# Performance work log

Measured on AMD Instinct MI355X. Metric: run time of the kernel, lower is better.

## Reference

```python
import jax, jax.numpy as jnp
import numpy as np

K = 5            # srn kernel size (kernels[0])
EPSILON = 1e-3   # epsilons -> SRN additive noise scale
BN_EPS = 1e-5
NUM_SLICES = 3
OUT_CH = 64
CLASSES = 5


def _unfold(x, k):
    # torch.nn.Unfold, padding=0: (B, C*k*k, L), channel-major then (kh, kw) row-major
    B, C, H, W = x.shape
    Ho, Wo = H - k + 1, W - k + 1
    cols = jnp.stack([x[:, :, i:i + Ho, j:j + Wo]
                      for i in range(k) for j in range(k)], axis=2)  # (B,C,k*k,Ho,Wo)
    return cols.reshape(B, C * k * k, Ho * Wo), Ho, Wo


def _bn(x, g, b):
    # BatchNorm2d in training mode: batch statistics, biased variance
    m = x.mean((0, 2, 3), keepdims=True)
    v = x.var((0, 2, 3), keepdims=True)
    return (x - m) * jax.lax.rsqrt(v + BN_EPS) * g[None, :, None, None] + b[None, :, None, None]


def _conv(x, w, b):
    y = jax.lax.conv_general_dilated(x, w, (1, 1), 'VALID',
                                     dimension_numbers=('NCHW', 'OIHW', 'NCHW'))
    return y + b[None, :, None, None]


def _avgpool(x, s):
    B, C, H, W = x.shape
    return x.reshape(B, C, H // s, s, W // s, s).mean((3, 5))


def _maxpool(x, s):
    B, C, H, W = x.shape
    return x.reshape(B, C, H // s, s, W // s, s).max((3, 5))


def _srn(x, srn_w):
    B = x.shape[0]
    y, Ho, Wo = _unfold(x, K)                               # (B, n, L)
    y = y + EPSILON * jax.random.normal(jax.random.key(42), y.shape, y.dtype)
    gg = jnp.std(y, axis=1, ddof=1, keepdims=True)          # torch.std is unbiased
    y = y / gg
    O, C, _, _, S = srn_w.shape
    n = C * K * K
    X = srn_w.reshape(O, n, S)
    X = jnp.concatenate([jnp.ones((O, n, 1), X.dtype), X], axis=2)   # (O, n, S+1)
    Xcov = jnp.einsum('onf,ong->ofg', X, X)                 # X^T X, (O, 4, 4)
    Xinv = jnp.linalg.inv(Xcov)
    M = jnp.einsum('ofg,ong->ofn', Xinv, X)
    Wc = jnp.einsum('ofn,bnl->bofl', M, y)
    pred = jnp.einsum('onf,bofl->bonl', X, Wc)              # fitted values (B,O,n,L)
    err = jnp.mean((y[:, None] - pred) ** 2, axis=2)        # (B,O,L)
    err = err.reshape(B, O, Ho, Wo)
    A = (jnp.exp(-err) - np.exp(-1.0)) / (1.0 - np.exp(-1.0))
    return A - 0.5


def setup_inputs() -> dict:
    key = jax.random.key(0)
    ks = jax.random.split(key, 12)
    x = jax.random.normal(ks[0], (4, 3, 64, 64), jnp.float32)
    # xavier-style init scaled up for numerical stability of the small-matrix inverse
    srn_w = 0.05 * jax.random.normal(ks[1], (OUT_CH, 3, K, K, NUM_SLICES), jnp.float32)
    conv2_w = 0.05 * jax.random.normal(ks[2], (128, 64, 3, 3), jnp.float32)
    conv2_b = 0.01 * jax.random.normal(ks[3], (128,), jnp.float32)
    conv3_w = 0.05 * jax.random.normal(ks[4], (128, 128, 3, 3), jnp.float32)
    conv3_b = 0.01 * jax.random.normal(ks[5], (128,), jnp.float32)
    conv4_w = 0.05 * jax.random.normal(ks[6], (128, 128, 3, 3), jnp.float32)
    conv4_b = 0.01 * jax.random.normal(ks[7], (128,), jnp.float32)
    bn1_g = jnp.ones((64,), jnp.float32); bn1_b = jnp.zeros((64,), jnp.float32)
    bn2_g = jnp.ones((128,), jnp.float32); bn2_b = jnp.zeros((128,), jnp.float32)
    bn3_g = jnp.ones((128,), jnp.float32); bn3_b = jnp.zeros((128,), jnp.float32)
    bn4_g = jnp.ones((128,), jnp.float32); bn4_b = jnp.zeros((128,), jnp.float32)
    fc2_w = 0.05 * jax.random.normal(ks[8], (CLASSES, 128, 1, 1), jnp.float32)
    fc2_b = 0.01 * jax.random.normal(ks[9], (CLASSES,), jnp.float32)
    return dict(x=x, srn_w=srn_w, conv2_w=conv2_w, conv2_b=conv2_b,
                conv3_w=conv3_w, conv3_b=conv3_b, conv4_w=conv4_w, conv4_b=conv4_b,
                bn1_g=bn1_g, bn1_b=bn1_b, bn2_g=bn2_g, bn2_b=bn2_b,
                bn3_g=bn3_g, bn3_b=bn3_b, bn4_g=bn4_g, bn4_b=bn4_b,
                fc2_w=fc2_w, fc2_b=fc2_b)


def reference(x, srn_w, conv2_w, conv2_b, conv3_w, conv3_b, conv4_w, conv4_b,
              bn1_g, bn1_b, bn2_g, bn2_b, bn3_g, bn3_b, bn4_g, bn4_b,
              fc2_w, fc2_b):
    h = _srn(x, srn_w)                                      # (B,64,60,60)
    h = _avgpool(h, 2)
    h = _bn(h, bn1_g, bn1_b)
    h = jax.nn.relu(_bn(_conv(h, conv2_w, conv2_b), bn2_g, bn2_b))
    h = _avgpool(h, 2)
    h = jax.nn.relu(_bn(_conv(h, conv3_w, conv3_b), bn3_g, bn3_b))
    h = _maxpool(h, 2)
    h = jax.nn.relu(_bn(_conv(h, conv4_w, conv4_b), bn4_g, bn4_b))
    h = _maxpool(h, 4)                                      # (B,128,1,1)
    flat = h.reshape(h.shape[0], -1)                        # (B,128)
    return flat @ fc2_w.reshape(CLASSES, -1).T + fc2_b      # 1x1 conv == matmul
```

## Files before the change

kernel.cpp:

```cpp
#include <hip/hip_runtime.h>
#include <math.h>

__device__ __align__(16) float g_w2p[9 * 2304 * 4];
__device__ __align__(16) float g_w3p[17 * 2304 * 4];
__device__ __align__(16) float g_w4p[8 * 4608 * 4];
__device__ __align__(16) float g_h1[4 * 30 * 30 * 64];
__device__ __align__(16) float g_h2[4 * 14 * 14 * 4 * 128];
__device__ __align__(16) float g_h3[4 * 6 * 6 * 4 * 128];
__device__ __align__(16) float g_h4[4 * 16 * 128];

__global__ __launch_bounds__(256) void k_srn(const float* __restrict__ x,
                                             const float* __restrict__ srn_w,
                                             const float* __restrict__ w2,
                                             float* __restrict__ stats) {
    __shared__ __align__(16) float wlds[64 * 244];
    __shared__ float xsm[648];
    __shared__ float part[2 * 15 * 66];
    __shared__ float redS[256], redQ[256];
    int bid = blockIdx.x, t = threadIdx.x;
    int b = bid / 60, rem = bid % 60, r = rem >> 1, ch = rem & 1;

    for (int j = bid * 256 + t; j < 73728; j += 240 * 256) {
        int c = j & 3, s4 = j >> 2;
        int sl = s4 % 36, tmp = s4 / 36, oc_l = tmp & 63, blk = tmp >> 6;
        int it = blk & 3, ocg = blk >> 2;
        int kw = sl % 3, icq = (sl / 3) & 3, kh = sl / 12;
        int ic = it * 16 + icq * 4 + c;
        g_w2p[j] = w2[((ocg * 64 + oc_l) * 64 + ic) * 9 + kh * 3 + kw];
    }

    float4 wr[15];
#pragma unroll
    for (int k = 0; k < 15; k++) {
        int i4 = k * 256 + t;
        if (i4 < 3600) wr[k] = ((const float4*)srn_w)[i4];
    }
    float xr[3];
#pragma unroll
    for (int k = 0; k < 3; k++) {
        int i = t + k * 256;
        if (i < 648) {
            int c = i / 216, rm = i % 216, rr = rm / 36, col = rm % 36;
            int gc = ch * 30 + col; if (gc > 63) gc = 63;
            xr[k] = x[((b * 3 + c) * 64 + (2 * r + rr)) * 64 + gc];
        }
    }
#pragma unroll
    for (int k = 0; k < 15; k++) {
        int i4 = k * 256 + t;
        if (i4 < 3600) {
            float v4[4] = { wr[k].x, wr[k].y, wr[k].z, wr[k].w };
#pragma unroll
            for (int e = 0; e < 4; e++) {
                int i = i4 * 4 + e, o = i / 225, jj = i % 225;
                wlds[o * 244 + (jj / 15) * 16 + (jj % 15)] = v4[e];
            }
        }
    }
#pragma unroll
    for (int k = 0; k < 3; k++) { int i = t + k * 256; if (i < 648) xsm[i] = xr[k]; }
    __syncthreads();

    int w = t >> 6, o = t & 63;
    int rw = w & 1, cq = w >> 1, base = cq * 16;

    float z1[16], z2[16], z3[16], s[16], q[16];
#pragma unroll
    for (int i = 0; i < 16; i++) { z1[i]=0; z2[i]=0; z3[i]=0; s[i]=0; q[i]=0; }

    for (int c = 0; c < 3; c++) {
#pragma unroll
        for (int kh = 0; kh < 5; kh++) {
            float xv[20];
#pragma unroll
            for (int k = 0; k < 20; k++) xv[k] = xsm[(c * 6 + rw + kh) * 36 + base + k];
            float wf[16];
            const float* wp = &wlds[o * 244 + (c * 5 + kh) * 16];
            *(float4*)&wf[0]  = *(const float4*)&wp[0];
            *(float4*)&wf[4]  = *(const float4*)&wp[4];
            *(float4*)&wf[8]  = *(const float4*)&wp[8];
            *(float4*)&wf[12] = *(const float4*)&wp[12];
#pragma unroll
            for (int kw = 0; kw < 5; kw++) {
                float w1 = wf[kw * 3], w2v = wf[kw * 3 + 1], w3v = wf[kw * 3 + 2];
#pragma unroll
                for (int i = 0; i < 16; i++) {
                    float v = xv[kw + i];
                    s[i] += v; q[i] += v * v;
                    z1[i] += w1 * v; z2[i] += w2v * v; z3[i] += w3v * v;
                }
            }
        }
    }

    float gm[16];
    {
        float c01=0,c02=0,c03=0,c11=0,c12=0,c13=0,c22=0,c23=0,c33=0;
#pragma unroll
        for (int row = 0; row < 15; row++) {
            float wf[16];
            const float* wp = &wlds[o * 244 + row * 16];
            *(float4*)&wf[0]  = *(const float4*)&wp[0];
            *(float4*)&wf[4]  = *(const float4*)&wp[4];
            *(float4*)&wf[8]  = *(const float4*)&wp[8];
            *(float4*)&wf[12] = *(const float4*)&wp[12];
#pragma unroll
            for (int kw = 0; kw < 5; kw++) {
                float w1 = wf[kw*3], w2v = wf[kw*3+1], w3v = wf[kw*3+2];
                c01 += w1; c02 += w2v; c03 += w3v;
                c11 += w1*w1; c12 += w1*w2v; c13 += w1*w3v;
                c22 += w2v*w2v; c23 += w2v*w3v; c33 += w3v*w3v;
            }
        }
        float A[4][8];
        A[0][0]=75.f; A[0][1]=c01; A[0][2]=c02; A[0][3]=c03;
        A[1][0]=c01;  A[1][1]=c11; A[1][2]=c12; A[1][3]=c13;
        A[2][0]=c02;  A[2][1]=c12; A[2][2]=c22; A[2][3]=c23;
        A[3][0]=c03;  A[3][1]=c13; A[3][2]=c23; A[3][3]=c33;
#pragma unroll
        for (int i = 0; i < 4; i++)
#pragma unroll
            for (int j = 0; j < 4; j++) A[i][4 + j] = (i == j) ? 1.f : 0.f;
#pragma unroll
        for (int p = 0; p < 4; p++) {
            float ip = 1.f / A[p][p];
#pragma unroll
            for (int j = 0; j < 8; j++) A[p][j] *= ip;
#pragma unroll
            for (int i = 0; i < 4; i++) if (i != p) {
                float f = A[i][p];
#pragma unroll
                for (int j = 0; j < 8; j++) A[i][j] -= f * A[p][j];
            }
        }
#pragma unroll
        for (int i = 0; i < 4; i++)
#pragma unroll
            for (int j = 0; j < 4; j++) gm[i * 4 + j] = A[i][4 + j];
    }

    const float C1 = 0.36787944117144233f;
    const float INV = 1.5819767068693265f;
#pragma unroll
    for (int pp = 0; pp < 8; pp++) {
        int pl = cq * 8 + pp;
        if (pl < 15) {
            float aa = 0.f;
#pragma unroll
            for (int e = 0; e < 2; e++) {
                int i = 2 * pp + e;
                float sum = s[i], sq = q[i];
                float gg2 = (sq - sum * sum * (1.f / 75.f)) * (1.f / 74.f);
                float zf[4] = { sum, z1[i], z2[i], z3[i] };
                float qf = 0.f;
#pragma unroll
                for (int f = 0; f < 4; f++) {
                    float acc = 0.f;
#pragma unroll
                    for (int h = 0; h < 4; h++) acc += gm[f * 4 + h] * zf[h];
                    qf += acc * zf[f];
                }
                float err = (sq - qf) / (75.f * gg2);
                aa += (expf(-err) - C1) * INV - 0.5f;
            }
            part[(rw * 15 + pl) * 66 + o] = 0.25f * aa;
        }
    }
    __syncthreads();

    int j2 = t >> 6;
    float ps = 0.f, pq = 0.f;
    for (int pl = j2; pl < 15; pl += 4) {
        float v = part[pl * 66 + o] + part[(15 + pl) * 66 + o];
        g_h1[((b * 30 + r) * 30 + ch * 15 + pl) * 64 + o] = v;
        ps += v; pq += v * v;
    }
    redS[t] = ps; redQ[t] = pq;
    __syncthreads();
    if (t < 64) {
        atomicAdd(&stats[t],      redS[t] + redS[64 + t] + redS[128 + t] + redS[192 + t]);
        atomicAdd(&stats[64 + t], redQ[t] + redQ[64 + t] + redQ[128 + t] + redQ[192 + t]);
    }
}

__global__ __launch_bounds__(256) void k_conv2(const float* __restrict__ w3,
                                               const float* __restrict__ g1,
                                               const float* __restrict__ b1,
                                               float* __restrict__ stats) {
    __shared__ __align__(16) float ws[64 * 148];
    __shared__ __align__(16) float xs[3 * 16 * 64];
    __shared__ float redS[256], redQ[256];
    int blk = blockIdx.x, t = threadIdx.x;
    int b = blk / 112, rem = blk % 112, oh = rem >> 2, sub = rem & 3;
    int owh = sub >> 1, ocg = sub & 1;
    int oc_l = t & 63, qtr = t >> 6;
    int now = (qtr < 2) ? 4 : 3;
    int lowb = (qtr < 2) ? qtr * 4 : 8 + (qtr - 2) * 3;

    for (int j = blk * 256 + t; j < 147456; j += 448 * 256) {
        int c = j & 3, s4 = j >> 2;
        int sl = s4 % 36, tmp = s4 / 36, oc2 = tmp & 63, bk = tmp >> 6;
        int it = bk & 7, og = bk >> 3;
        int kw = sl % 3, icq = (sl / 3) & 3, kh = sl / 12;
        int ic = it * 16 + icq * 4 + c;
        g_w3p[j] = w3[((og * 64 + oc2) * 128 + ic) * 9 + kh * 3 + kw];
    }

    {
        int icb = (t & 15) * 4;
        float4 S = *(const float4*)&stats[icb], Q = *(const float4*)&stats[64 + icb];
        float4 G4 = *(const float4*)&g1[icb], B4 = *(const float4*)&b1[icb];
        float scv[4], shv[4];
        float mm[4] = { S.x, S.y, S.z, S.w }, qq[4] = { Q.x, Q.y, Q.z, Q.w };
        float gg[4] = { G4.x, G4.y, G4.z, G4.w }, bb[4] = { B4.x, B4.y, B4.z, B4.w };
#pragma unroll
        for (int c = 0; c < 4; c++) {
            float m = mm[c] * (1.f / 3600.f);
            float v = qq[c] * (1.f / 3600.f) - m * m;
            scv[c] = gg[c] * rsqrtf(v + 1e-5f);
            shv[c] = bb[c] - m * scv[c];
        }
        int px = t >> 4, ic4 = t & 15;
        float4 xr[3];
#pragma unroll
        for (int k = 0; k < 3; k++)
            xr[k] = ((const float4*)g_h1)[((b * 30 + oh + k) * 30 + owh * 14 + px) * 16 + ic4];
        const float4* wsrc0 = (const float4*)g_w2p;
        float4 wreg[9];
#pragma unroll
        for (int k = 0; k < 9; k++) wreg[k] = wsrc0[(ocg * 4) * 2304 + k * 256 + t];
#pragma unroll
        for (int k = 0; k < 3; k++) {
            float4 v;
            v.x = xr[k].x * scv[0] + shv[0]; v.y = xr[k].y * scv[1] + shv[1];
            v.z = xr[k].z * scv[2] + shv[2]; v.w = xr[k].w * scv[3] + shv[3];
            *(float4*)&xs[((k * 16 + px) * 16 + ic4) * 4] = v;
        }
#pragma unroll
        for (int k = 0; k < 9; k++) {
            int idx = k * 256 + t;
            *(float4*)&ws[(idx / 36) * 148 + (idx % 36) * 4] = wreg[k];
        }
    }
    __syncthreads();

    float acc[4] = {0, 0, 0, 0};
    const float4* wsrc = (const float4*)g_w2p + (ocg * 4) * 2304;
    for (int it = 0; it < 4; ++it) {
        float4 wreg[9];
        if (it < 3) {
#pragma unroll
            for (int k = 0; k < 9; k++) wreg[k] = wsrc[(it + 1) * 2304 + k * 256 + t];
        }
#pragma unroll 1
        for (int icq = 0; icq < 4; icq++) {
            int xoff = it * 16 + icq * 4;
#pragma unroll
            for (int kh = 0; kh < 3; kh++) {
                const float* wb = &ws[oc_l * 148 + (kh * 4 + icq) * 12];
                float4 w0 = *(const float4*)&wb[0];
                float4 w1 = *(const float4*)&wb[4];
                float4 w2v = *(const float4*)&wb[8];
                const float* xrow = &xs[(kh * 16 + lowb) * 64 + xoff];
                float4 x0 = *(const float4*)&xrow[0];
                float4 x1 = *(const float4*)&xrow[64];
#pragma unroll
                for (int i = 0; i < 4; i++) {
                    if (i < now) {
                        float4 x2 = *(const float4*)&xrow[(i + 2) * 64];
                        acc[i] += w0.x * x0.x + w0.y * x0.y + w0.z * x0.z + w0.w * x0.w
                                + w1.x * x1.x + w1.y * x1.y + w1.z * x1.z + w1.w * x1.w
                                + w2v.x * x2.x + w2v.y * x2.y + w2v.z * x2.z + w2v.w * x2.w;
                        x0 = x1; x1 = x2;
                    }
                }
            }
        }
        if (it < 3) {
            __syncthreads();
#pragma unroll
            for (int k = 0; k < 9; k++) {
                int idx = k * 256 + t;
                *(float4*)&ws[(idx / 36) * 148 + (idx % 36) * 4] = wreg[k];
            }
            __syncthreads();
        }
    }
    int oc = ocg * 64 + oc_l;
    float ps = 0.f, pq = 0.f;
#pragma unroll
    for (int i = 0; i < 4; i++) {
        if (i < now) {
            int ow = owh * 14 + lowb + i;
            g_h2[(((b * 14 + (oh >> 1)) * 14 + (ow >> 1)) * 4 + (oh & 1) * 2 + (ow & 1)) * 128 + oc] = acc[i];
            ps += acc[i]; pq += acc[i] * acc[i];
        }
    }
    redS[t] = ps; redQ[t] = pq;
    __syncthreads();
    if (t < 64) {
        atomicAdd(&stats[128 + ocg * 64 + t], redS[t] + redS[64 + t] + redS[128 + t] + redS[192 + t]);
        atomicAdd(&stats[256 + ocg * 64 + t], redQ[t] + redQ[64 + t] + redQ[128 + t] + redQ[192 + t]);
    }
}

__global__ __launch_bounds__(256) void k_conv3(const float* __restrict__ w4,
                                               const float* __restrict__ g2,
                                               const float* __restrict__ b2,
                                               float* __restrict__ stats) {
    __shared__ __align__(16) float ws[64 * 148];
    __shared__ __align__(16) float xs[3 * 8 * 128];
    __shared__ float redS[256], redQ[256];
    int blk = blockIdx.x, t = threadIdx.x;
    int b = blk / 48, rem = blk % 48, oh = rem >> 2, sub = rem & 3;
    int owh = sub >> 1, ocg = sub & 1;
    int oc_l = t & 63, qtr = t >> 6;
    int now = (qtr < 2) ? 2 : 1;
    int lowb = (qtr < 2) ? qtr * 2 : 4 + (qtr - 2);

    for (int j = blk * 256 + t; j < 147456; j += 192 * 256) {
        int c = j & 3, s4 = j >> 2;
        int sl = s4 % 72, tmp = s4 / 72, oc2 = tmp & 15, blkq = tmp >> 4;
        int icq = blkq & 3, og = blkq >> 2;
        int kw = sl % 3, icb2 = (sl / 3) & 7, kh = sl / 24;
        int ic = icq * 32 + icb2 * 4 + c;
        g_w4p[j] = w4[((og * 16 + oc2) * 128 + ic) * 9 + kh * 3 + kw];
    }

    {
        int icb = (t & 31) * 4;
        float4 S = *(const float4*)&stats[128 + icb], Q = *(const float4*)&stats[256 + icb];
        float4 G4 = *(const float4*)&g2[icb], B4 = *(const float4*)&b2[icb];
        float scv[4], shv[4];
        float mm[4] = { S.x, S.y, S.z, S.w }, qq[4] = { Q.x, Q.y, Q.z, Q.w };
        float gg[4] = { G4.x, G4.y, G4.z, G4.w }, bb[4] = { B4.x, B4.y, B4.z, B4.w };
#pragma unroll
        for (int c = 0; c < 4; c++) {
            float m = mm[c] * (1.f / 3136.f);
            float v = qq[c] * (1.f / 3136.f) - m * m;
            scv[c] = gg[c] * rsqrtf(v + 1e-5f);
            shv[c] = bb[c] - m * scv[c];
        }
        const float4* wsrc0 = (const float4*)g_w3p;
        float4 wreg[9];
#pragma unroll
        for (int k = 0; k < 9; k++) wreg[k] = wsrc0[(ocg * 8) * 2304 + k * 256 + t];
        int px = (t >> 5) & 7, ic4 = t & 31;
        float4 pa[3], pb[3], pc[3], pd[3];
#pragma unroll
        for (int k = 0; k < 3; k++) {
            const float4* p0 = (const float4*)&g_h2[(((b * 14 + oh + k) * 14 + owh * 6 + px) * 4) * 128 + ic4 * 4];
            pa[k] = p0[0]; pb[k] = p0[32]; pc[k] = p0[64]; pd[k] = p0[96];
        }
#pragma unroll
        for (int k = 0; k < 9; k++) {
            int idx = k * 256 + t;
            *(float4*)&ws[(idx / 36) * 148 + (idx % 36) * 4] = wreg[k];
        }
#pragma unroll
        for (int k = 0; k < 3; k++) {
            float4 o4;
            o4.x = 0.25f * (fmaxf(pa[k].x * scv[0] + shv[0], 0.f) + fmaxf(pb[k].x * scv[0] + shv[0], 0.f)
                          + fmaxf(pc[k].x * scv[0] + shv[0], 0.f) + fmaxf(pd[k].x * scv[0] + shv[0], 0.f));
            o4.y = 0.25f * (fmaxf(pa[k].y * scv[1] + shv[1], 0.f) + fmaxf(pb[k].y * scv[1] + shv[1], 0.f)
                          + fmaxf(pc[k].y * scv[1] + shv[1], 0.f) + fmaxf(pd[k].y * scv[1] + shv[1], 0.f));
            o4.z = 0.25f * (fmaxf(pa[k].z * scv[2] + shv[2], 0.f) + fmaxf(pb[k].z * scv[2] + shv[2], 0.f)
                          + fmaxf(pc[k].z * scv[2] + shv[2], 0.f) + fmaxf(pd[k].z * scv[2] + shv[2], 0.f));
            o4.w = 0.25f * (fmaxf(pa[k].w * scv[3] + shv[3], 0.f) + fmaxf(pb[k].w * scv[3] + shv[3], 0.f)
                          + fmaxf(pc[k].w * scv[3] + shv[3], 0.f) + fmaxf(pd[k].w * scv[3] + shv[3], 0.f));
            *(float4*)&xs[((k * 8 + px) * 32 + ic4) * 4] = o4;
        }
    }
    __syncthreads();

    float acc[2] = {0, 0};
    const float4* wsrc = (const float4*)g_w3p + (ocg * 8) * 2304;
    for (int it = 0; it < 8; ++it) {
        float4 wreg[9];
        if (it < 7) {
#pragma unroll
            for (int k = 0; k < 9; k++) wreg[k] = wsrc[(it + 1) * 2304 + k * 256 + t];
        }
#pragma unroll 1
        for (int icq = 0; icq < 4; icq++) {
            int xoff = it * 16 + icq * 4;
#pragma unroll
            for (int kh = 0; kh < 3; kh++) {
                const float* wb = &ws[oc_l * 148 + (kh * 4 + icq) * 12];
                float4 w0 = *(const float4*)&wb[0];
                float4 w1 = *(const float4*)&wb[4];
                float4 w2v = *(const float4*)&wb[8];
                const float* xrow = &xs[(kh * 8 + lowb) * 128 + xoff];
                float4 x0 = *(const float4*)&xrow[0];
                float4 x1 = *(const float4*)&xrow[128];
#pragma unroll
                for (int i = 0; i < 2; i++) {
                    if (i < now) {
                        float4 x2 = *(const float4*)&xrow[(i + 2) * 128];
                        acc[i] += w0.x * x0.x + w0.y * x0.y + w0.z * x0.z + w0.w * x0.w
                                + w1.x * x1.x + w1.y * x1.y + w1.z * x1.z + w1.w * x1.w
                                + w2v.x * x2.x + w2v.y * x2.y + w2v.z * x2.z + w2v.w * x2.w;
                        x0 = x1; x1 = x2;
                    }
                }
            }
        }
        if (it < 7) {
            __syncthreads();
#pragma unroll
            for (int k = 0; k < 9; k++) {
                int idx = k * 256 + t;
                *(float4*)&ws[(idx / 36) * 148 + (idx % 36) * 4] = wreg[k];
            }
            __syncthreads();
        }
    }
    int oc = ocg * 64 + oc_l;
    float ps = 0.f, pq = 0.f;
#pragma unroll
    for (int i = 0; i < 2; i++) {
        if (i < now) {
            int ow = owh * 6 + lowb + i;
            g_h3[(((b * 6 + (oh >> 1)) * 6 + (ow >> 1)) * 4 + (oh & 1) * 2 + (ow & 1)) * 128 + oc] = acc[i];
            ps += acc[i]; pq += acc[i] * acc[i];
        }
    }
    redS[t] = ps; redQ[t] = pq;
    __syncthreads();
    if (t < 64) {
        atomicAdd(&stats[384 + ocg * 64 + t], redS[t] + redS[64 + t] + redS[128 + t] + redS[192 + t]);
        atomicAdd(&stats[512 + ocg * 64 + t], redQ[t] + redQ[64 + t] + redQ[128 + t] + redQ[192 + t]);
    }
}

__global__ __launch_bounds__(256) void k_conv4(const float* __restrict__ g3,
                                               const float* __restrict__ b3,
                                               float* __restrict__ stats) {
    __shared__ __align__(16) float ws[64 * 292];
    __shared__ __align__(16) float xs[3 * 6 * 128];
    __shared__ float red[256];
    int blk = blockIdx.x, t = threadIdx.x;
    int b = blk / 32, rem = blk % 32, oh = rem / 8, ocg = rem % 8;
    int oc_l = t & 15, ow = (t >> 4) & 3, icq = t >> 6;

    {
        int icb = (t & 31) * 4;
        float4 S = *(const float4*)&stats[384 + icb], Q = *(const float4*)&stats[512 + icb];
        float4 G4 = *(const float4*)&g3[icb], B4 = *(const float4*)&b3[icb];
        float scv[4], shv[4];
        float mm[4] = { S.x, S.y, S.z, S.w }, qq[4] = { Q.x, Q.y, Q.z, Q.w };
        float gg[4] = { G4.x, G4.y, G4.z, G4.w }, bb[4] = { B4.x, B4.y, B4.z, B4.w };
#pragma unroll
        for (int c = 0; c < 4; c++) {
            float m = mm[c] * (1.f / 576.f);
            float v = qq[c] * (1.f / 576.f) - m * m;
            scv[c] = gg[c] * rsqrtf(v + 1e-5f);
            shv[c] = bb[c] - m * scv[c];
        }
        const float4* wsrc = (const float4*)g_w4p + ocg * 4608;
        float4 wreg[18];
#pragma unroll
        for (int k = 0; k < 18; k++) wreg[k] = wsrc[k * 256 + t];
        float4 pa[3], pb[3], pc[3], pd[3];
#pragma unroll
        for (int k = 0; k < 3; k++) {
            int i4 = t + k * 256;
            if (i4 < 576) {
                int px = (i4 >> 5) % 6, rr = i4 / 192;
                const float4* p0 = (const float4*)&g_h3[(((b * 6 + oh + rr) * 6 + px) * 4) * 128 + (i4 & 31) * 4];
                pa[k] = p0[0]; pb[k] = p0[32]; pc[k] = p0[64]; pd[k] = p0[96];
            }
        }
#pragma unroll
        for (int k = 0; k < 18; k++) {
            int idx = k * 256 + t;
            *(float4*)&ws[(idx / 72) * 292 + (idx % 72) * 4] = wreg[k];
        }
#pragma unroll
        for (int k = 0; k < 3; k++) {
            int i4 = t + k * 256;
            if (i4 < 576) {
                float4 o4;
                o4.x = fmaxf(fmaxf(fmaxf(pa[k].x * scv[0] + shv[0], pb[k].x * scv[0] + shv[0]),
                                   fmaxf(pc[k].x * scv[0] + shv[0], pd[k].x * scv[0] + shv[0])), 0.f);
                o4.y = fmaxf(fmaxf(fmaxf(pa[k].y * scv[1] + shv[1], pb[k].y * scv[1] + shv[1]),
                                   fmaxf(pc[k].y * scv[1] + shv[1], pd[k].y * scv[1] + shv[1])), 0.f);
                o4.z = fmaxf(fmaxf(fmaxf(pa[k].z * scv[2] + shv[2], pb[k].z * scv[2] + shv[2]),
                                   fmaxf(pc[k].z * scv[2] + shv[2], pd[k].z * scv[2] + shv[2])), 0.f);
                o4.w = fmaxf(fmaxf(fmaxf(pa[k].w * scv[3] + shv[3], pb[k].w * scv[3] + shv[3]),
                                   fmaxf(pc[k].w * scv[3] + shv[3], pd[k].w * scv[3] + shv[3])), 0.f);
                *(float4*)&xs[i4 * 4] = o4;
            }
        }
    }
    __syncthreads();

    float acc = 0.f;
    const float* wbase = &ws[(icq * 16 + oc_l) * 292];
#pragma unroll 1
    for (int icbq = 0; icbq < 8; icbq++) {
#pragma unroll
        for (int kh = 0; kh < 3; kh++) {
            const float* wb = &wbase[(kh * 8 + icbq) * 12];
            float4 w0 = *(const float4*)&wb[0];
            float4 w1 = *(const float4*)&wb[4];
            float4 w2v = *(const float4*)&wb[8];
            float4 x0 = *(const float4*)&xs[(kh * 6 + ow) * 128 + icq * 32 + icbq * 4];
            float4 x1 = *(const float4*)&xs[(kh * 6 + ow + 1) * 128 + icq * 32 + icbq * 4];
            float4 x2 = *(const float4*)&xs[(kh * 6 + ow + 2) * 128 + icq * 32 + icbq * 4];
            acc += w0.x * x0.x + w0.y * x0.y + w0.z * x0.z + w0.w * x0.w
                 + w1.x * x1.x + w1.y * x1.y + w1.z * x1.z + w1.w * x1.w
                 + w2v.x * x2.x + w2v.y * x2.y + w2v.z * x2.z + w2v.w * x2.w;
        }
    }
    red[t] = acc;
    __syncthreads();
    if (t < 64) {
        float v = red[t] + red[t + 64] + red[t + 128] + red[t + 192];
        int oc = ocg * 16 + (t & 15);
        g_h4[((b * 4 + oh) * 4 + (t >> 4)) * 128 + oc] = v;
        float ps = v + __shfl_xor(v, 16);  ps += __shfl_xor(ps, 32);
        float pv = v * v;
        float pq = pv + __shfl_xor(pv, 16); pq += __shfl_xor(pq, 32);
        if (t < 16) {
            atomicAdd(&stats[640 + ocg * 16 + t], ps);
            atomicAdd(&stats[768 + ocg * 16 + t], pq);
        }
    }
}

__global__ __launch_bounds__(256) void k_final(const float* __restrict__ g4,
                                               const float* __restrict__ b4,
                                               const float* __restrict__ fcw,
                                               const float* __restrict__ fcb,
                                               const float* __restrict__ stats,
                                               float* __restrict__ out) {
    __shared__ float sc[128], sh[128];
    __shared__ float pooled[4][128];
    int t = threadIdx.x;
    if (t < 128) {
        float m = stats[640 + t] * (1.f / 64.f);
        float v = stats[768 + t] * (1.f / 64.f) - m * m;
        float rs = rsqrtf(v + 1e-5f);
        sc[t] = g4[t] * rs; sh[t] = b4[t] - m * sc[t];
    }
    __syncthreads();
    for (int item = t; item < 512; item += 256) {
        int bb = item >> 7, oc = item & 127;
        float s = sc[oc], h = sh[oc];
        float mx = 0.f;
#pragma unroll
        for (int k = 0; k < 16; k++) mx = fmaxf(mx, g_h4[(bb * 16 + k) * 128 + oc] * s + h);
        pooled[bb][oc] = mx;
    }
    __syncthreads();
    if (t < 20) {
        int bb = t / 5, cls = t % 5;
        float acc = fcb[cls];
        const float* w = &fcw[cls * 128];
        for (int oc = 0; oc < 128; oc++) acc += pooled[bb][oc] * w[oc];
        out[bb * 5 + cls] = acc;
    }
}

extern "C" void kernel_launch(void* const* d_in, const int* in_sizes, int n_in,
                              void* d_out, int out_size, void* d_ws, size_t ws_size,
                              hipStream_t stream) {
    (void)in_sizes; (void)n_in; (void)out_size; (void)ws_size;
    const float* x     = (const float*)d_in[0];
    const float* srn_w = (const float*)d_in[1];
    const float* w2    = (const float*)d_in[2];
    const float* w3    = (const float*)d_in[4];
    const float* w4    = (const float*)d_in[6];
    const float* g1 = (const float*)d_in[8];  const float* b1 = (const float*)d_in[9];
    const float* g2 = (const float*)d_in[10]; const float* b2 = (const float*)d_in[11];
    const float* g3 = (const float*)d_in[12]; const float* b3 = (const float*)d_in[13];
    const float* g4 = (const float*)d_in[14]; const float* b4 = (const float*)d_in[15];
    const float* fcw = (const float*)d_in[16]; const float* fcb = (const float*)d_in[17];
    float* out = (float*)d_out;
    float* stats = (float*)d_ws;

    hipMemsetAsync(d_ws, 0, 4096, stream);
    k_srn  <<<dim3(240), dim3(256), 0, stream>>>(x, srn_w, w2, stats);
    k_conv2<<<dim3(448), dim3(256), 0, stream>>>(w3, g1, b1, stats);
    k_conv3<<<dim3(192), dim3(256), 0, stream>>>(w4, g2, b2, stats);
    k_conv4<<<dim3(128), dim3(256), 0, stream>>>(g3, b3, stats);
    k_final<<<dim3(1),   dim3(256), 0, stream>>>(g4, b4, fcw, fcb, stats, out);
}
```

Before: 113.7 us.

## Repartition conv2/conv3 blocks to 32 output channels with two-tile weight staging

Conv2 and conv3 now give each block 32 output channels instead of 64, with 8 thread groups each covering 1-2 output columns. Conv2 doubles its grid to 896 blocks, and conv3 covers the full output row per block. Weight packing is changed to match, and each refill stages two 16-input-channel tiles in shared memory, which halves the number of barrier/refill rounds. This raises parallelism and occupancy, but lowers the work per thread and reuse of each loaded weight.

```diff
diff --git a/kernel.cpp b/kernel.cpp
--- a/kernel.cpp
+++ b/kernel.cpp
@@ -1,8 +1,8 @@
 #include <hip/hip_runtime.h>
 #include <math.h>
 
-__device__ __align__(16) float g_w2p[9 * 2304 * 4];
-__device__ __align__(16) float g_w3p[17 * 2304 * 4];
+__device__ __align__(16) float g_w2p[16 * 1152 * 4];
+__device__ __align__(16) float g_w3p[32 * 1152 * 4];
 __device__ __align__(16) float g_w4p[8 * 4608 * 4];
 __device__ __align__(16) float g_h1[4 * 30 * 30 * 64];
 __device__ __align__(16) float g_h2[4 * 14 * 14 * 4 * 128];
@@ -22,11 +22,11 @@
 
     for (int j = bid * 256 + t; j < 73728; j += 240 * 256) {
         int c = j & 3, s4 = j >> 2;
-        int sl = s4 % 36, tmp = s4 / 36, oc_l = tmp & 63, blk = tmp >> 6;
+        int sl = s4 % 36, tmp = s4 / 36, oc_l = tmp & 31, blk = tmp >> 5;
         int it = blk & 3, ocg = blk >> 2;
         int kw = sl % 3, icq = (sl / 3) & 3, kh = sl / 12;
         int ic = it * 16 + icq * 4 + c;
-        g_w2p[j] = w2[((ocg * 64 + oc_l) * 64 + ic) * 9 + kh * 3 + kw];
+        g_w2p[j] = w2[((ocg * 32 + oc_l) * 64 + ic) * 9 + kh * 3 + kw];
     }
 
     float4 wr[15];
@@ -187,25 +187,29 @@
                                                const float* __restrict__ g1,
                                                const float* __restrict__ b1,
                                                float* __restrict__ stats) {
-    __shared__ __align__(16) float ws[64 * 148];
+    __shared__ __align__(16) float ws[2 * 32 * 148];
     __shared__ __align__(16) float xs[3 * 16 * 64];
     __shared__ float redS[256], redQ[256];
     int blk = blockIdx.x, t = threadIdx.x;
-    int b = blk / 112, rem = blk % 112, oh = rem >> 2, sub = rem & 3;
-    int owh = sub >> 1, ocg = sub & 1;
-    int oc_l = t & 63, qtr = t >> 6;
-    int now = (qtr < 2) ? 4 : 3;
-    int lowb = (qtr < 2) ? qtr * 4 : 8 + (qtr - 2) * 3;
-
-    for (int j = blk * 256 + t; j < 147456; j += 448 * 256) {
-        int c = j & 3, s4 = j >> 2;
-        int sl = s4 % 36, tmp = s4 / 36, oc2 = tmp & 63, bk = tmp >> 6;
-        int it = bk & 7, og = bk >> 3;
-        int kw = sl % 3, icq = (sl / 3) & 3, kh = sl / 12;
-        int ic = it * 16 + icq * 4 + c;
-        g_w3p[j] = w3[((og * 64 + oc2) * 128 + ic) * 9 + kh * 3 + kw];
-    }
-
+    int b = blk / 224, rem = blk % 224, oh = rem >> 3, sub = rem & 7;
+    int owh = sub >> 2, ocg = sub & 3;
+    int oc_l = t & 31, grp = t >> 5;
+    int now = (grp < 6) ? 2 : 1;
+    int lowb = (grp < 6) ? grp * 2 : 12 + (grp - 6);
+
+    {
+        int j = blk * 256 + t;
+        if (j < 147456) {
+            int c = j & 3, s4 = j >> 2;
+            int sl = s4 % 36, tmp = s4 / 36, oc2 = tmp & 31, bk = tmp >> 5;
+            int it = bk & 7, og = bk >> 3;
+            int kw = sl % 3, icq = (sl / 3) & 3, kh = sl / 12;
+            int ic = it * 16 + icq * 4 + c;
+            g_w3p[j] = w3[((og * 32 + oc2) * 128 + ic) * 9 + kh * 3 + kw];
+        }
+    }
+
+    const float4* wsrc = (const float4*)g_w2p + (ocg * 4) * 1152;
     {
         int icb = (t & 15) * 4;
         float4 S = *(const float4*)&stats[icb], Q = *(const float4*)&stats[64 + icb];
@@ -225,10 +229,9 @@
 #pragma unroll
         for (int k = 0; k < 3; k++)
             xr[k] = ((const float4*)g_h1)[((b * 30 + oh + k) * 30 + owh * 14 + px) * 16 + ic4];
-        const float4* wsrc0 = (const float4*)g_w2p;
         float4 wreg[9];
 #pragma unroll
-        for (int k = 0; k < 9; k++) wreg[k] = wsrc0[(ocg * 4) * 2304 + k * 256 + t];
+        for (int k = 0; k < 9; k++) wreg[k] = wsrc[k * 256 + t];
 #pragma unroll
         for (int k = 0; k < 3; k++) {
             float4 v;
@@ -239,57 +242,62 @@
 #pragma unroll
         for (int k = 0; k < 9; k++) {
             int idx = k * 256 + t;
-            *(float4*)&ws[(idx / 36) * 148 + (idx % 36) * 4] = wreg[k];
-        }
-    }
-    __syncthreads();
-
-    float acc[4] = {0, 0, 0, 0};
-    const float4* wsrc = (const float4*)g_w2p + (ocg * 4) * 2304;
-    for (int it = 0; it < 4; ++it) {
+            int tile = idx / 1152, r2 = idx % 1152;
+            *(float4*)&ws[tile * 4736 + (r2 / 36) * 148 + (r2 % 36) * 4] = wreg[k];
+        }
+    }
+    __syncthreads();
+
+    float acc[2] = {0, 0};
+    for (int rr = 0; rr < 2; ++rr) {
         float4 wreg[9];
-        if (it < 3) {
-#pragma unroll
-            for (int k = 0; k < 9; k++) wreg[k] = wsrc[(it + 1) * 2304 + k * 256 + t];
-        }
+        if (rr == 0) {
+#pragma unroll
+            for (int k = 0; k < 9; k++) wreg[k] = wsrc[2 * 1152 + k * 256 + t];
+        }
+        for (int half = 0; half < 2; ++half) {
+            int it = rr * 2 + half;
+            const float* wB = &ws[half * 4736 + oc_l * 148];
 #pragma unroll 1
-        for (int icq = 0; icq < 4; icq++) {
-            int xoff = it * 16 + icq * 4;
-#pragma unroll
-            for (int kh = 0; kh < 3; kh++) {
-                const float* wb = &ws[oc_l * 148 + (kh * 4 + icq) * 12];
-                float4 w0 = *(const float4*)&wb[0];
-                float4 w1 = *(const float4*)&wb[4];
-                float4 w2v = *(const float4*)&wb[8];
-                const float* xrow = &xs[(kh * 16 + lowb) * 64 + xoff];
-                float4 x0 = *(const float4*)&xrow[0];
-                float4 x1 = *(const float4*)&xrow[64];
-#pragma unroll
-                for (int i = 0; i < 4; i++) {
-                    if (i < now) {
-                        float4 x2 = *(const float4*)&xrow[(i + 2) * 64];
-                        acc[i] += w0.x * x0.x + w0.y * x0.y + w0.z * x0.z + w0.w * x0.w
-                                + w1.x * x1.x + w1.y * x1.y + w1.z * x1.z + w1.w * x1.w
-                                + w2v.x * x2.x + w2v.y * x2.y + w2v.z * x2.z + w2v.w * x2.w;
-                        x0 = x1; x1 = x2;
+            for (int icq = 0; icq < 4; icq++) {
+                int xoff = it * 16 + icq * 4;
+#pragma unroll
+                for (int kh = 0; kh < 3; kh++) {
+                    const float* wb = &wB[(kh * 4 + icq) * 12];
+                    float4 w0 = *(const float4*)&wb[0];
+                    float4 w1 = *(const float4*)&wb[4];
+                    float4 w2v = *(const float4*)&wb[8];
+                    const float* xrow = &xs[(kh * 16 + lowb) * 64 + xoff];
+                    float4 x0 = *(const float4*)&xrow[0];
+                    float4 x1 = *(const float4*)&xrow[64];
+#pragma unroll
+                    for (int i = 0; i < 2; i++) {
+                        if (i < now) {
+                            float4 x2 = *(const float4*)&xrow[(i + 2) * 64];
+                            acc[i] += w0.x * x0.x + w0.y * x0.y + w0.z * x0.z + w0.w * x0.w
+                                    + w1.x * x1.x + w1.y * x1.y + w1.z * x1.z + w1.w * x1.w
+                                    + w2v.x * x2.x + w2v.y * x2.y + w2v.z * x2.z + w2v.w * x2.w;
+                            x0 = x1; x1 = x2;
+                        }
                     }
                 }
             }
         }
-        if (it < 3) {
+        if (rr == 0) {
             __syncthreads();
 #pragma unroll
             for (int k = 0; k < 9; k++) {
                 int idx = k * 256 + t;
-                *(float4*)&ws[(idx / 36) * 148 + (idx % 36) * 4] = wreg[k];
+                int tile = idx / 1152, r2 = idx % 1152;
+                *(float4*)&ws[tile * 4736 + (r2 / 36) * 148 + (r2 % 36) * 4] = wreg[k];
             }
             __syncthreads();
         }
     }
-    int oc = ocg * 64 + oc_l;
+    int oc = ocg * 32 + oc_l;
     float ps = 0.f, pq = 0.f;
 #pragma unroll
-    for (int i = 0; i < 4; i++) {
+    for (int i = 0; i < 2; i++) {
         if (i < now) {
             int ow = owh * 14 + lowb + i;
             g_h2[(((b * 14 + (oh >> 1)) * 14 + (ow >> 1)) * 4 + (oh & 1) * 2 + (ow & 1)) * 128 + oc] = acc[i];
@@ -298,9 +306,12 @@
     }
     redS[t] = ps; redQ[t] = pq;
     __syncthreads();
-    if (t < 64) {
-        atomicAdd(&stats[128 + ocg * 64 + t], redS[t] + redS[64 + t] + redS[128 + t] + redS[192 + t]);
-        atomicAdd(&stats[256 + ocg * 64 + t], redQ[t] + redQ[64 + t] + redQ[128 + t] + redQ[192 + t]);
+    if (t < 32) {
+        float aS = 0.f, aQ = 0.f;
+#pragma unroll
+        for (int k = 0; k < 8; k++) { aS += redS[t + 32 * k]; aQ += redQ[t + 32 * k]; }
+        atomicAdd(&stats[128 + ocg * 32 + t], aS);
+        atomicAdd(&stats[256 + ocg * 32 + t], aQ);
     }
 }
 
@@ -308,15 +319,14 @@
                                                const float* __restrict__ g2,
                                                const float* __restrict__ b2,
                                                float* __restrict__ stats) {
-    __shared__ __align__(16) float ws[64 * 148];
-    __shared__ __align__(16) float xs[3 * 8 * 128];
+    __shared__ __align__(16) float ws[2 * 32 * 148];
+    __shared__ __align__(16) float xs[3 * 14 * 128];
     __shared__ float redS[256], redQ[256];
     int blk = blockIdx.x, t = threadIdx.x;
-    int b = blk / 48, rem = blk % 48, oh = rem >> 2, sub = rem & 3;
-    int owh = sub >> 1, ocg = sub & 1;
-    int oc_l = t & 63, qtr = t >> 6;
-    int now = (qtr < 2) ? 2 : 1;
-    int lowb = (qtr < 2) ? qtr * 2 : 4 + (qtr - 2);
+    int b = blk / 48, rem = blk % 48, oh = rem >> 2, ocg = rem & 3;
+    int oc_l = t & 31, grp = t >> 5;
+    int now = (grp < 4) ? 2 : 1;
+    int lowb = (grp < 4) ? grp * 2 : 8 + (grp - 4);
 
     for (int j = blk * 256 + t; j < 147456; j += 192 * 256) {
         int c = j & 3, s4 = j >> 2;
@@ -327,6 +337,7 @@
         g_w4p[j] = w4[((og * 16 + oc2) * 128 + ic) * 9 + kh * 3 + kw];
     }
 
+    const float4* wsrc = (const float4*)g_w3p + (ocg * 8) * 1152;
     {
         int icb = (t & 31) * 4;
         float4 S = *(const float4*)&stats[128 + icb], Q = *(const float4*)&stats[256 + icb];
@@ -341,95 +352,108 @@
             scv[c] = gg[c] * rsqrtf(v + 1e-5f);
             shv[c] = bb[c] - m * scv[c];
         }
-        const float4* wsrc0 = (const float4*)g_w3p;
         float4 wreg[9];
 #pragma unroll
-        for (int k = 0; k < 9; k++) wreg[k] = wsrc0[(ocg * 8) * 2304 + k * 256 + t];
-        int px = (t >> 5) & 7, ic4 = t & 31;
-        float4 pa[3], pb[3], pc[3], pd[3];
-#pragma unroll
-        for (int k = 0; k < 3; k++) {
-            const float4* p0 = (const float4*)&g_h2[(((b * 14 + oh + k) * 14 + owh * 6 + px) * 4) * 128 + ic4 * 4];
-            pa[k] = p0[0]; pb[k] = p0[32]; pc[k] = p0[64]; pd[k] = p0[96];
+        for (int k = 0; k < 9; k++) wreg[k] = wsrc[k * 256 + t];
+        float4 pa[6], pb[6], pc[6], pd[6];
+#pragma unroll
+        for (int k = 0; k < 6; k++) {
+            int i4 = t + k * 256;
+            if (i4 < 1344) {
+                int px = (i4 >> 5) % 14, rr2 = i4 / 448;
+                const float4* p0 = (const float4*)&g_h2[(((b * 14 + oh + rr2) * 14 + px) * 4) * 128 + (i4 & 31) * 4];
+                pa[k] = p0[0]; pb[k] = p0[32]; pc[k] = p0[64]; pd[k] = p0[96];
+            }
         }
 #pragma unroll
         for (int k = 0; k < 9; k++) {
             int idx = k * 256 + t;
-            *(float4*)&ws[(idx / 36) * 148 + (idx % 36) * 4] = wreg[k];
-        }
-#pragma unroll
-        for (int k = 0; k < 3; k++) {
-            float4 o4;
-            o4.x = 0.25f * (fmaxf(pa[k].x * scv[0] + shv[0], 0.f) + fmaxf(pb[k].x * scv[0] + shv[0], 0.f)
-                          + fmaxf(pc[k].x * scv[0] + shv[0], 0.f) + fmaxf(pd[k].x * scv[0] + shv[0], 0.f));
-            o4.y = 0.25f * (fmaxf(pa[k].y * scv[1] + shv[1], 0.f) + fmaxf(pb[k].y * scv[1] + shv[1], 0.f)
-                          + fmaxf(pc[k].y * scv[1] + shv[1], 0.f) + fmaxf(pd[k].y * scv[1] + shv[1], 0.f));
-            o4.z = 0.25f * (fmaxf(pa[k].z * scv[2] + shv[2], 0.f) + fmaxf(pb[k].z * scv[2] + shv[2], 0.f)
-                          + fmaxf(pc[k].z * scv[2] + shv[2], 0.f) + fmaxf(pd[k].z * scv[2] + shv[2], 0.f));
-            o4.w = 0.25f * (fmaxf(pa[k].w * scv[3] + shv[3], 0.f) + fmaxf(pb[k].w * scv[3] + shv[3], 0.f)
-                          + fmaxf(pc[k].w * scv[3] + shv[3], 0.f) + fmaxf(pd[k].w * scv[3] + shv[3], 0.f));
-            *(float4*)&xs[((k * 8 + px) * 32 + ic4) * 4] = o4;
+            int tile = idx / 1152, r2 = idx % 1152;
+            *(float4*)&ws[tile * 4736 + (r2 / 36) * 148 + (r2 % 36) * 4] = wreg[k];
+        }
+#pragma unroll
+        for (int k = 0; k < 6; k++) {
+            int i4 = t + k * 256;
+            if (i4 < 1344) {
+                float4 o4;
+                o4.x = 0.25f * (fmaxf(pa[k].x * scv[0] + shv[0], 0.f) + fmaxf(pb[k].x * scv[0] + shv[0], 0.f)
+                              + fmaxf(pc[k].x * scv[0] + shv[0], 0.f) + fmaxf(pd[k].x * scv[0] + shv[0], 0.f));
+                o4.y = 0.25f * (fmaxf(pa[k].y * scv[1] + shv[1], 0.f) + fmaxf(pb[k].y * scv[1] + shv[1], 0.f)
+                              + fmaxf(pc[k].y * scv[1] + shv[1], 0.f) + fmaxf(pd[k].y * scv[1] + shv[1], 0.f));
+                o4.z = 0.25f * (fmaxf(pa[k].z * scv[2] + shv[2], 0.f) + fmaxf(pb[k].z * scv[2] + shv[2], 0.f)
+                              + fmaxf(pc[k].z * scv[2] + shv[2], 0.f) + fmaxf(pd[k].z * scv[2] + shv[2], 0.f));
+                o4.w = 0.25f * (fmaxf(pa[k].w * scv[3] + shv[3], 0.f) + fmaxf(pb[k].w * scv[3] + shv[3], 0.f)
+                              + fmaxf(pc[k].w * scv[3] + shv[3], 0.f) + fmaxf(pd[k].w * scv[3] + shv[3], 0.f));
+                *(float4*)&xs[i4 * 4] = o4;
+            }
         }
     }
     __syncthreads();
 
     float acc[2] = {0, 0};
-    const float4* wsrc = (const float4*)g_w3p + (ocg * 8) * 2304;
-    for (int it = 0; it < 8; ++it) {
+    for (int rr = 0; rr < 4; ++rr) {
         float4 wreg[9];
-        if (it < 7) {
-#pragma unroll
-            for (int k = 0; k < 9; k++) wreg[k] = wsrc[(it + 1) * 2304 + k * 256 + t];
-        }
+        if (rr < 3) {
+#pragma unroll
+            for (int k = 0; k < 9; k++) wreg[k] = wsrc[(2 * rr + 2) * 1152 + k * 256 + t];
+        }
+        for (int half = 0; half < 2; ++half) {
+            int it = rr * 2 + half;
+            const float* wB = &ws[half * 4736 + oc_l * 148];
 #pragma unroll 1
-        for (int icq = 0; icq < 4; icq++) {
-            int xoff = it * 16 + icq * 4;
-#pragma unroll
-            for (int kh = 0; kh < 3; kh++) {
-                const float* wb = &ws[oc_l * 148 + (kh * 4 + icq) * 12];
-                float4 w0 = *(const float4*)&wb[0];
-                float4 w1 = *(const float4*)&wb[4];
-                float4 w2v = *(const float4*)&wb[8];
-                const float* xrow = &xs[(kh * 8 + lowb) * 128 + xoff];
-                float4 x0 = *(const float4*)&xrow[0];
-                float4 x1 = *(const float4*)&xrow[128];
-#pragma unroll
-                for (int i = 0; i < 2; i++) {
-                    if (i < now) {
-                        float4 x2 = *(const float4*)&xrow[(i + 2) * 128];
-                        acc[i] += w0.x * x0.x + w0.y * x0.y + w0.z * x0.z + w0.w * x0.w
-                                + w1.x * x1.x + w1.y * x1.y + w1.z * x1.z + w1.w * x1.w
-                                + w2v.x * x2.x + w2v.y * x2.y + w2v.z * x2.z + w2v.w * x2.w;
-                        x0 = x1; x1 = x2;
+            for (int icq = 0; icq < 4; icq++) {
+                int xoff = it * 16 + icq * 4;
+#pragma unroll
+                for (int kh = 0; kh < 3; kh++) {
+                    const float* wb = &wB[(kh * 4 + icq) * 12];
+                    float4 w0 = *(const float4*)&wb[0];
+                    float4 w1 = *(const float4*)&wb[4];
+                    float4 w2v = *(const float4*)&wb[8];
+                    const float* xrow = &xs[(kh * 14 + lowb) * 128 + xoff];
+                    float4 x0 = *(const float4*)&xrow[0];
+                    float4 x1 = *(const float4*)&xrow[128];
+#pragma unroll
+                    for (int i = 0; i < 2; i++) {
+                        if (i < now) {
+                            float4 x2 = *(const float4*)&xrow[(i + 2) * 128];
+                            acc[i] += w0.x * x0.x + w0.y * x0.y + w0.z * x0.z + w0.w * x0.w
+                                    + w1.x * x1.x + w1.y * x1.y + w1.z * x1.z + w1.w * x1.w
+                                    + w2v.x * x2.x + w2v.y * x2.y + w2v.z * x2.z + w2v.w * x2.w;
+                            x0 = x1; x1 = x2;
+                        }
                     }
                 }
             }
         }
-        if (it < 7) {
+        if (rr < 3) {
             __syncthreads();
 #pragma unroll
             for (int k = 0; k < 9; k++) {
                 int idx = k * 256 + t;
-                *(float4*)&ws[(idx / 36) * 148 + (idx % 36) * 4] = wreg[k];
+                int tile = idx / 1152, r2 = idx % 1152;
+                *(float4*)&ws[tile * 4736 + (r2 / 36) * 148 + (r2 % 36) * 4] = wreg[k];
             }
             __syncthreads();
         }
     }
-    int oc = ocg * 64 + oc_l;
+    int oc = ocg * 32 + oc_l;
     float ps = 0.f, pq = 0.f;
 #pragma unroll
     for (int i = 0; i < 2; i++) {
         if (i < now) {
-            int ow = owh * 6 + lowb + i;
+            int ow = lowb + i;
             g_h3[(((b * 6 + (oh >> 1)) * 6 + (ow >> 1)) * 4 + (oh & 1) * 2 + (ow & 1)) * 128 + oc] = acc[i];
             ps += acc[i]; pq += acc[i] * acc[i];
         }
     }
     redS[t] = ps; redQ[t] = pq;
     __syncthreads();
-    if (t < 64) {
-        atomicAdd(&stats[384 + ocg * 64 + t], redS[t] + redS[64 + t] + redS[128 + t] + redS[192 + t]);
-        atomicAdd(&stats[512 + ocg * 64 + t], redQ[t] + redQ[64 + t] + redQ[128 + t] + redQ[192 + t]);
+    if (t < 32) {
+        float aS = 0.f, aQ = 0.f;
+#pragma unroll
+        for (int k = 0; k < 8; k++) { aS += redS[t + 32 * k]; aQ += redQ[t + 32 * k]; }
+        atomicAdd(&stats[384 + ocg * 32 + t], aS);
+        atomicAdd(&stats[512 + ocg * 32 + t], aQ);
     }
 }
 
@@ -582,7 +606,7 @@
 
     hipMemsetAsync(d_ws, 0, 4096, stream);
     k_srn  <<<dim3(240), dim3(256), 0, stream>>>(x, srn_w, w2, stats);
-    k_conv2<<<dim3(448), dim3(256), 0, stream>>>(w3, g1, b1, stats);
+    k_conv2<<<dim3(896), dim3(256), 0, stream>>>(w3, g1, b1, stats);
     k_conv3<<<dim3(192), dim3(256), 0, stream>>>(w4, g2, b2, stats);
     k_conv4<<<dim3(128), dim3(256), 0, stream>>>(g3, b3, stats);
     k_final<<<dim3(1),   dim3(256), 0, stream>>>(g4, b4, fcw, fcb, stats, out);
```

Result: faster. 102.3 us (-10.1%).
